# Optimization experiments

Measured on AMD Instinct MI355X. Metric: run time of the kernel, lower is better.

The kernel has to match this reference:

```python
import jax, jax.numpy as jnp
import numpy as np

NF = 96   # out_channel_M
G = 8     # deformable groups
K = 3     # deform conv kernel size


def conv2d(x, w, b, stride=1, pad=1):
    out = jax.lax.conv_general_dilated(x, w, (stride, stride), [(pad, pad), (pad, pad)],
                                       dimension_numbers=('NCHW', 'OIHW', 'NCHW'))
    return out + b[None, :, None, None]


def conv_transpose2d(x, w, b, stride=2, pad=1, out_pad=1):
    # PyTorch ConvTranspose2d semantics; w is [Cin, Cout, k, k]
    k = w.shape[2]
    wt = jnp.flip(w, (2, 3)).transpose(1, 0, 2, 3)  # -> OIHW
    p = (k - 1 - pad, k - 1 - pad + out_pad)
    out = jax.lax.conv_general_dilated(x, wt, (1, 1), [p, p], lhs_dilation=(stride, stride),
                                       dimension_numbers=('NCHW', 'OIHW', 'NCHW'))
    return out + b[None, :, None, None]


def lrelu(x):
    return jax.nn.leaky_relu(x, 0.1)


def deform_conv(x, offset, w, b):
    """DCNv1: offset-driven bilinear sampling + 3x3 contraction (stride=1, pad=1).
    x: [B,C,H,W], offset: [B, 2*G*K*K, H, W] (per-group (dy,dx) interleaved per tap)."""
    B, C, H, W = x.shape
    K2 = K * K
    Cg = C // G
    off = offset.reshape(B, G, K2, 2, H, W)
    ky, kx = jnp.meshgrid(jnp.arange(K), jnp.arange(K), indexing='ij')
    # sampling positions: p = p0 + p_k + delta_p  (zero padding of 1)
    py = (jnp.arange(H, dtype=x.dtype)[None, None, None, :, None]
          + (ky.reshape(K2) - 1).astype(x.dtype)[None, None, :, None, None] + off[:, :, :, 0])
    px = (jnp.arange(W, dtype=x.dtype)[None, None, None, None, :]
          + (kx.reshape(K2) - 1).astype(x.dtype)[None, None, :, None, None] + off[:, :, :, 1])
    y0 = jnp.floor(py); x0 = jnp.floor(px)
    ly = py - y0; lx = px - x0
    y0i = y0.astype(jnp.int32); x0i = x0.astype(jnp.int32)
    xg = x.reshape(B, G, Cg, H * W)  # channels within a deformable group share offsets

    def gather(yi, xi):
        valid = ((yi >= 0) & (yi < H) & (xi >= 0) & (xi < W)).astype(x.dtype)  # [B,G,K2,H,W]
        idx = jnp.clip(yi, 0, H - 1) * W + jnp.clip(xi, 0, W - 1)
        g = jnp.take_along_axis(xg, idx.reshape(B, G, 1, K2 * H * W), axis=3)
        return g.reshape(B, G, Cg, K2, H, W) * valid[:, :, None]

    bw = lambda a: a[:, :, None]  # broadcast bilinear weight over channel axis
    v = (gather(y0i, x0i) * bw((1 - ly) * (1 - lx))
         + gather(y0i, x0i + 1) * bw((1 - ly) * lx)
         + gather(y0i + 1, x0i) * bw(ly * (1 - lx))
         + gather(y0i + 1, x0i + 1) * bw(ly * lx))
    sampled = v.reshape(B, C, K2, H, W)
    out = jnp.einsum('bckhw,ock->bohw', sampled, w.reshape(w.shape[0], C, K2))
    return out + b[None, :, None, None]


def setup_inputs():
    key = jax.random.key(0)
    ks = jax.random.split(key, 16)
    B, H, W = 2, 128, 128
    s = 0.05
    wgt = lambda k, shape: jax.random.normal(k, shape, jnp.float32) * s
    return {
        'ref_fea': jax.random.normal(ks[0], (B, NF, H, W), jnp.float32),
        'inp_fea': jax.random.normal(ks[1], (B, NF, H, W), jnp.float32),
        'oc1_w': wgt(ks[2], (NF, 2 * NF, 3, 3)), 'oc1_b': jnp.zeros((NF,), jnp.float32),
        'oc3_w': wgt(ks[3], (NF, NF, 3, 3)), 'oc3_b': jnp.zeros((NF,), jnp.float32),
        'enc1_w': wgt(ks[4], (NF, NF, 3, 3)), 'enc1_b': jnp.zeros((NF,), jnp.float32),
        'enc2_w': wgt(ks[5], (NF, NF, 3, 3)), 'enc2_b': jnp.zeros((NF,), jnp.float32),
        'dec1_w': wgt(ks[6], (NF, NF, 3, 3)), 'dec1_b': jnp.zeros((NF,), jnp.float32),
        'dec2_w': wgt(ks[7], (NF, NF, 3, 3)), 'dec2_b': jnp.zeros((NF,), jnp.float32),
        'coff_w': wgt(ks[8], (2 * G * K * K, NF, 3, 3)), 'coff_b': jnp.zeros((2 * G * K * K,), jnp.float32),
        'dcn_w': wgt(ks[9], (NF, NF, 3, 3)), 'dcn_b': jnp.zeros((NF,), jnp.float32),
        'ref1_w': wgt(ks[10], (NF, 2 * NF, 3, 3)), 'ref1_b': jnp.zeros((NF,), jnp.float32),
        'ref2_w': wgt(ks[11], (NF, NF, 3, 3)), 'ref2_b': jnp.zeros((NF,), jnp.float32),
    }


def reference(ref_fea, inp_fea, oc1_w, oc1_b, oc3_w, oc3_b, enc1_w, enc1_b, enc2_w, enc2_b,
              dec1_w, dec1_b, dec2_w, dec2_b, coff_w, coff_b, dcn_w, dcn_b,
              ref1_w, ref1_b, ref2_w, ref2_b):
    # MotionEstimation
    t = jnp.concatenate([ref_fea, inp_fea], axis=1)
    t = lrelu(conv2d(t, oc1_w, oc1_b))
    t = lrelu(conv2d(t, oc3_w, oc3_b))
    en_offset = conv2d(lrelu(conv2d(t, enc1_w, enc1_b, stride=2)), enc2_w, enc2_b, stride=2)
    # Q: round-to-integer quantization (straight-through; same forward value as round)
    q_offset = en_offset + jax.lax.stop_gradient(jnp.round(en_offset) - en_offset)
    # MotionCompensation
    de_offset = conv_transpose2d(lrelu(conv_transpose2d(q_offset, dec1_w, dec1_b)), dec2_w, dec2_b)
    offset = conv2d(de_offset, coff_w, coff_b)  # conv_offset inside DCNv1 (extra_offset_mask)
    aligned = deform_conv(ref_fea, offset, dcn_w, dcn_b)
    r = lrelu(conv2d(jnp.concatenate([aligned, ref_fea], axis=1), ref1_w, ref1_b))
    r = lrelu(conv2d(r, ref2_w, ref2_b))
    return aligned + r, en_offset, q_offset
```

## Files before the change

### kernel.cpp

```cpp
#include <hip/hip_runtime.h>
#include <hip/hip_bf16.h>

typedef __hip_bfloat16 bf16;
typedef __attribute__((ext_vector_type(8))) short s8;
typedef __attribute__((ext_vector_type(4))) short s4;
typedef __attribute__((ext_vector_type(4))) float f4;

#define N_FEA   3145728
#define N_EN    196608
#define N_E1    786432
#define OUT_EN  3145728
#define OUT_Q   3342336

__device__ __forceinline__ float b2f(bf16 v) { return __bfloat162float(v); }
__device__ __forceinline__ float bs2f(short v) {
    union { unsigned u; float f; } x; x.u = ((unsigned)(unsigned short)v) << 16; return x.f;
}

__global__ void wpack_sw(const float* __restrict__ w1, const float* __restrict__ w3,
                         float* __restrict__ o1, float* __restrict__ o3) {
    long i = (long)blockIdx.x * 256 + threadIdx.x;
    const long n1 = 2L * 12 * 96 * 72;
    if (i < n1) {
        int ky = (int)(i % 3); long t = i / 3;
        int o = (int)(t % 8); t /= 8;
        int kx = (int)(t % 3); t /= 3;
        int c = (int)(t % 96); t /= 96;
        int ocg = (int)(t % 12); int ks = (int)(t / 12);
        o1[i] = w1[((long)(ocg * 8 + o) * 192 + ks * 96 + c) * 9 + ky * 3 + kx];
        return;
    }
    i -= n1;
    const long n3 = 2L * 12 * 48 * 72;
    if (i < n3) {
        int ky = (int)(i % 3); long t = i / 3;
        int o = (int)(t % 8); t /= 8;
        int kx = (int)(t % 3); t /= 3;
        int c = (int)(t % 48); t /= 48;
        int ocg = (int)(t % 12); int ks = (int)(t / 12);
        o3[i] = w3[((long)(ocg * 8 + o) * 96 + ks * 48 + c) * 9 + ky * 3 + kx];
    }
}

__global__ void wpack_enc(const float* __restrict__ w1, const float* __restrict__ w2,
                          float* __restrict__ o1, float* __restrict__ o2) {
    long i = (long)blockIdx.x * 256 + threadIdx.x;
    const long n1 = 24L * 96 * 4 * 9;
    if (i < n1) {
        int k = (int)(i % 9);
        int o = (int)((i / 9) % 4);
        int c = (int)((i / 36) % 96);
        int ocg = (int)(i / (36 * 96));
        o1[i] = w1[((long)(ocg * 4 + o) * 96 + c) * 9 + k];
        return;
    }
    i -= n1;
    const long n2 = 48L * 96 * 2 * 9;
    if (i < n2) {
        int k = (int)(i % 9);
        int o = (int)((i / 9) % 2);
        int c = (int)((i / 18) % 96);
        int ocg = (int)(i / (18 * 96));
        o2[i] = w2[((long)(ocg * 2 + o) * 96 + c) * 9 + k];
    }
}

template <int OCB>
__global__ __launch_bounds__(256) void conv3x3_sw(
    const float* __restrict__ inA, int cA, int bstrA,
    const float* __restrict__ inB, int cB, int bstrB,
    const float* __restrict__ wsc,
    float* __restrict__ P0, float* __restrict__ P1, int Cout) {
    const int H = 128, W = 128;
    const int NOC = Cout / OCB;
    int bid = blockIdx.x;
    const int ks = bid & 1;
    int r = bid >> 1;
    const int strip = r & 15; r >>= 4;
    const int ocg = r % NOC;
    const int b = r / NOC;
    const float* in = ks ? inB : inA;
    const int cN = ks ? cB : cA;
    const int bstr = ks ? bstrB : bstrA;
    float* P = ks ? P1 : P0;
    const float* wq0 = wsc + ((long)(ks * NOC + ocg) * cN) * 72;

    const int ox = threadIdx.x & 127;
    const int ry = (threadIdx.x >> 7) << 2;
    const int oy0 = strip * 8 + ry;
    const int iyb = oy0 - 1;

    bool vy[6];
#pragma unroll
    for (int j = 0; j < 6; ++j) vy[j] = (unsigned)(iyb + j) < (unsigned)H;

    float acc[OCB][4];
#pragma unroll
    for (int o = 0; o < OCB; ++o)
#pragma unroll
        for (int j = 0; j < 4; ++j) acc[o][j] = 0.f;

    const float* pc = in + (long)b * bstr * H * W + (long)iyb * W;
    for (int c = 0; c < cN; ++c) {
        const float* wq = wq0 + c * 72;
#pragma unroll
        for (int kx = 0; kx < 3; ++kx) {
            const int ix = ox + kx - 1;
            const bool vx = (unsigned)ix < (unsigned)W;
            float rv[6];
#pragma unroll
            for (int j = 0; j < 6; ++j)
                rv[j] = (vx && vy[j]) ? pc[j * W + ix] : 0.f;
#pragma unroll
            for (int o = 0; o < OCB; ++o) {
#pragma unroll
                for (int ky = 0; ky < 3; ++ky) {
                    float wz = wq[kx * 24 + o * 3 + ky];
#pragma unroll
                    for (int j = 0; j < 4; ++j)
                        acc[o][j] = fmaf(rv[j + ky], wz, acc[o][j]);
                }
            }
        }
        pc += (long)H * W;
    }
#pragma unroll
    for (int o = 0; o < OCB; ++o) {
        long base = (((long)b * Cout + ocg * OCB + o) * H + oy0) * W + ox;
#pragma unroll
        for (int j = 0; j < 4; ++j) P[base + (long)j * W] = acc[o][j];
    }
}

__global__ void fuse_add_k(const float* __restrict__ p0, const float* __restrict__ p1,
                           const float* __restrict__ bias, float* __restrict__ out) {
    long idx = (long)blockIdx.x * 256 + threadIdx.x;
    if (idx >= (long)N_FEA) return;
    int oc = (int)((idx >> 14) % 96);
    float a = bias[oc] + p0[idx] + p1[idx];
    out[idx] = a > 0.f ? a : 0.1f * a;
}

template <int OCB>
__global__ __launch_bounds__(256) void conv_s2_px(
    const float* __restrict__ in, int Cin, int Hin, int Win,
    const float* __restrict__ wsc, const float* __restrict__ bias,
    float* __restrict__ out, int Cout, int relu,
    float* __restrict__ qq, float* __restrict__ qf2) {
    const int Hout = Hin >> 1, Wout = Win >> 1;
    const int rpb = 256 / Wout;
    const int strips = Hout / rpb;
    int bid = blockIdx.x;
    const int strip = bid % strips; bid /= strips;
    const int NOC = Cout / OCB;
    const int ocg = bid % NOC;
    const int b = bid / NOC;
    const int tid = threadIdx.x;
    const int ox = tid % Wout;
    const int oy = strip * rpb + tid / Wout;
    const int iy0 = oy * 2 - 1, ix0 = ox * 2 - 1;
    const float* wq0 = wsc + (long)(ocg * Cin) * (OCB * 9);

    float acc[OCB];
#pragma unroll
    for (int o = 0; o < OCB; ++o) acc[o] = bias[ocg * OCB + o];
    const bool vx0 = ix0 >= 0;
    const bool vy0 = iy0 >= 0;

    const float* pc = in + (long)b * Cin * Hin * Win + (long)iy0 * Win + ix0;
    for (int c = 0; c < Cin; ++c) {
        float rv[3][3];
#pragma unroll
        for (int jr = 0; jr < 3; ++jr) {
            const float* row = pc + jr * Win;
            const bool vr = jr ? true : vy0;
            rv[jr][0] = (vr && vx0) ? row[0] : 0.f;
            rv[jr][1] = vr ? row[1] : 0.f;
            rv[jr][2] = vr ? row[2] : 0.f;
        }
        const float* wq = wq0 + c * (OCB * 9);
#pragma unroll
        for (int o = 0; o < OCB; ++o)
#pragma unroll
            for (int ky = 0; ky < 3; ++ky)
#pragma unroll
                for (int kx = 0; kx < 3; ++kx)
                    acc[o] = fmaf(rv[ky][kx], wq[o * 9 + ky * 3 + kx], acc[o]);
        pc += (long)Hin * Win;
    }
#pragma unroll
    for (int o = 0; o < OCB; ++o) {
        long idx = (((long)b * Cout + ocg * OCB + o) * Hout + oy) * Wout + ox;
        float a = acc[o];
        if (relu) a = a > 0.f ? a : 0.1f * a;
        out[idx] = a;
        if (qq) {
            float qv = rintf(a);
            qq[idx] = qv;
            qf2[idx] = qv;
        }
    }
}

template <int HWC>
__global__ __launch_bounds__(256) void convt3x3_v2(
    const float* __restrict__ in, const float* __restrict__ w,
    const float* __restrict__ bias, void* __restrict__ out,
    int Hin, int Win, int relu) {
    const int C = 96;
    const int Hout = 2 * Hin, Wout = 2 * Win;
    const int strips = (Hout * Wout) / 1024;
    int bid = blockIdx.x;
    const int strip = bid % strips; bid /= strips;
    const int oc = bid % C;
    const int b = bid / C;
    __shared__ float wl[864];
    for (int i = threadIdx.x; i < C * 9; i += 256) {
        int c = i / 9, k = i % 9;
        wl[i] = w[((long)c * C + oc) * 9 + k];
    }
    __syncthreads();
    const int pix = strip * 1024 + threadIdx.x * 4;
    const int oy = pix / Wout, oxb = pix % Wout;
    const int c0x = oxb >> 1;
    const int oyE = oy + 1;
    float acc[4];
    const float bz = bias[oc];
#pragma unroll
    for (int j = 0; j < 4; ++j) acc[j] = bz;
    const bool r2ok = (c0x + 2) < Win;

    const float* pl = in + (long)b * C * Hin * Win;
    for (int c = 0; c < C; ++c) {
        float wv[9];
#pragma unroll
        for (int k = 0; k < 9; ++k) wv[k] = wl[c * 9 + k];
#pragma unroll
        for (int ky = 0; ky < 3; ++ky) {
            int ty = oyE - ky;
            if (ty & 1) continue;
            int iy = ty >> 1;
            if ((unsigned)iy >= (unsigned)Hin) continue;
            const float* row = pl + (long)iy * Win + c0x;
            float r0 = row[0];
            float r1 = row[1];
            float r2 = r2ok ? row[2] : 0.f;
            acc[0] = fmaf(r0, wv[ky * 3 + 1], acc[0]);
            acc[1] = fmaf(r1, wv[ky * 3 + 0], acc[1]);
            acc[1] = fmaf(r0, wv[ky * 3 + 2], acc[1]);
            acc[2] = fmaf(r1, wv[ky * 3 + 1], acc[2]);
            acc[3] = fmaf(r2, wv[ky * 3 + 0], acc[3]);
            acc[3] = fmaf(r1, wv[ky * 3 + 2], acc[3]);
        }
        pl += (long)Hin * Win;
    }
#pragma unroll
    for (int j = 0; j < 4; ++j) {
        float a = acc[j];
        if (relu) a = a > 0.f ? a : 0.1f * a;
        if (HWC)
            ((bf16*)out)[((long)b * Hout * Wout + oy * Wout + oxb + j) * 96 + oc] =
                __float2bfloat16(a);
        else
            ((float*)out)[(((long)b * C + oc) * Hout + oy) * Wout + oxb + j] = a;
    }
}

__device__ __forceinline__ void packw(const float* __restrict__ w, bf16* __restrict__ wP,
                                      int Cin, int swap, long i) {
    const int cpt = Cin >> 5;
    int e = (int)(i & 7);
    int n16 = (int)((i >> 3) & 15);
    int q = (int)((i >> 7) & 3);
    long t = i >> 9;
    int ci = (int)(t % cpt); t /= cpt;
    int tap = (int)(t % 9);
    int g = (int)(t / 9);
    int oc = g * 16 + n16;
    int c = ci * 32 + q * 8 + e;
    int cs = swap ? (c + Cin / 2) % Cin : c;
    wP[i] = __float2bfloat16(w[((long)oc * Cin + cs) * 9 + tap]);
}
__global__ void wxform_all(const float* __restrict__ coffw, const float* __restrict__ ref1w,
                           const float* __restrict__ ref2w, const float* __restrict__ dcnw,
                           bf16* __restrict__ p_coff, bf16* __restrict__ p_ref1,
                           bf16* __restrict__ p_ref2, bf16* __restrict__ p_dcn) {
    const long n1 = 124416, n2 = 165888, n3 = 82944, n4 = 82944;
    long i = (long)blockIdx.x * 256 + threadIdx.x;
    if (i < n1) { packw(coffw, p_coff, 96, 0, i); return; }
    i -= n1;
    if (i < n2) { packw(ref1w, p_ref1, 192, 1, i); return; }
    i -= n2;
    if (i < n3) { packw(ref2w, p_ref2, 96, 0, i); return; }
    i -= n3;
    if (i < n4) {
        int e = (int)(i & 7);
        int n16 = (int)((i >> 3) & 15);
        int q = (int)((i >> 7) & 3);
        long t = i >> 9;
        int ci = (int)(t % 27);
        int g = (int)(t / 27);
        int kp = ci * 32 + q * 8 + e;
        int c = kp % 96, kk = kp / 96;
        p_dcn[i] = __float2bfloat16(dcnw[(long)(g * 16 + n16) * 864 + c * 9 + kk]);
    }
}

__global__ void pack_hwc(const float* __restrict__ src, bf16* __restrict__ dst,
                         int HW, int Cs, int coff) {
    long i = (long)blockIdx.x * 256 + threadIdx.x;
    if (i >= 2L * 96 * HW) return;
    int px = (int)(i % HW);
    long t = i / HW;
    int c = (int)(t % 96);
    int b = (int)(t / 96);
    dst[((long)b * HW + px) * Cs + coff + c] = __float2bfloat16(src[i]);
}

template <int EPI>
__global__ __launch_bounds__(256) void mconv(
    const bf16* __restrict__ X, const bf16* __restrict__ wP,
    const float* __restrict__ bias, void* __restrict__ out,
    const bf16* __restrict__ res,
    int Cin, int Cout, int H, int W, int relu) {
    const int HW = H * W;
    const int NG = Cout >> 4, split = (NG + 1) >> 1;
    int bid = blockIdx.x;
    const int nb = HW >> 6;
    const int pxb = (bid % nb) << 6;
    const int b = bid / nb;
    const int wave = threadIdx.x >> 6, lane = threadIdx.x & 63;
    const int mt = (wave >> 1) << 5;
    const int og0 = (wave & 1) ? split : 0;
    const int og1 = (wave & 1) ? NG : split;
    const int q = lane >> 4, n16 = lane & 15;
    const int pA0 = pxb + mt + n16, pA1 = pA0 + 16;
    const int oy0 = pA0 / W, ox0 = pA0 % W;
    const int oy1 = pA1 / W, ox1 = pA1 % W;
    const long ib = (long)b * HW * Cin;
    f4 acc0[5], acc1[5];
    const f4 z4 = {0.f, 0.f, 0.f, 0.f};
#pragma unroll
    for (int g = 0; g < 5; ++g) { acc0[g] = z4; acc1[g] = z4; }
    const s8 z8 = {0, 0, 0, 0, 0, 0, 0, 0};
    const int cpt = Cin >> 5;
    const int lofs = lane << 3;
    for (int tap = 0; tap < 9; ++tap) {
        const int ky = tap / 3 - 1, kx = tap % 3 - 1;
        const int iy0 = oy0 + ky, ix0 = ox0 + kx;
        const int iy1 = oy1 + ky, ix1 = ox1 + kx;
        const bool v0 = (unsigned)iy0 < (unsigned)H && (unsigned)ix0 < (unsigned)W;
        const bool v1 = (unsigned)iy1 < (unsigned)H && (unsigned)ix1 < (unsigned)W;
        const bf16* pa0 = X + ib + ((long)iy0 * W + ix0) * Cin + q * 8;
        const bf16* pa1 = X + ib + ((long)iy1 * W + ix1) * Cin + q * 8;
        for (int ci = 0; ci < cpt; ++ci) {
            const int c0 = ci << 5;
            s8 a0 = v0 ? *(const s8*)(pa0 + c0) : z8;
            s8 a1 = v1 ? *(const s8*)(pa1 + c0) : z8;
#pragma unroll
            for (int gi = 0; gi < 5; ++gi) {
                int g = og0 + gi;
                if (g >= og1) break;
                s8 bb = *(const s8*)(wP + ((long)(g * 9 + tap) * cpt + ci) * 512 + lofs);
                acc0[gi] = __builtin_amdgcn_mfma_f32_16x16x32_bf16(a0, bb, acc0[gi], 0, 0, 0);
                acc1[gi] = __builtin_amdgcn_mfma_f32_16x16x32_bf16(a1, bb, acc1[gi], 0, 0, 0);
            }
        }
    }
#pragma unroll
    for (int gi = 0; gi < 5; ++gi) {
        int g = og0 + gi;
        if (g >= og1) break;
        int oc = g * 16 + n16;
        float bz = bias[oc];
#pragma unroll
        for (int t = 0; t < 2; ++t) {
            f4 a = t ? acc1[gi] : acc0[gi];
            int pxl = pxb + mt + t * 16 + q * 4;
#pragma unroll
            for (int r = 0; r < 4; ++r) {
                float v = a[r] + bz;
                if (relu) v = v > 0.f ? v : 0.1f * v;
                int px = pxl + r;
                if (EPI == 0)
                    ((bf16*)out)[((long)b * HW + px) * Cout + oc] = __float2bfloat16(v);
                else {
                    v += b2f(res[((long)b * HW + px) * 192 + 96 + oc]);
                    ((float*)out)[((long)b * Cout + oc) * HW + px] = v;
                }
            }
        }
    }
}

__global__ __launch_bounds__(256, 4) void deform_m_k(
    const bf16* __restrict__ Xref, const bf16* __restrict__ offs,
    const bf16* __restrict__ wD, const float* __restrict__ db,
    bf16* __restrict__ X2) {
    const int H = 128, W = 128;
    __shared__ bf16 offL[16 * 144];
    __shared__ bf16 s[16][872];
    int bid = blockIdx.x;
    const int band = bid & 7;
    int r = bid >> 3;
    const int b = r >> 7; r &= 127;
    const int rowin = r >> 3, xb = r & 7;
    const int oy = band * 16 + rowin;
    const int ox0 = xb * 16;
    const int tid = threadIdx.x;
    const long pxbase = (long)b * (H * W) + oy * W + ox0;
    for (int e = tid; e < 16 * 144; e += 256)
        offL[e] = offs[(pxbase + (e / 144)) * 144 + (e % 144)];
    __syncthreads();
    const long refb = (long)b * (H * W);
    for (int e = tid; e < 16 * 72; e += 256) {
        int p = e / 72, rem = e % 72;
        int g8 = rem / 9, kk = rem % 9;
        int ox = ox0 + p;
        float offy = b2f(offL[p * 144 + g8 * 18 + kk * 2]);
        float offx = b2f(offL[p * 144 + g8 * 18 + kk * 2 + 1]);
        float py = (float)(oy + kk / 3 - 1) + offy;
        float px = (float)(ox + kk % 3 - 1) + offx;
        float y0f = floorf(py), x0f = floorf(px);
        float ly = py - y0f, lx = px - x0f;
        int y0 = (int)y0f, x0 = (int)x0f;
        float w00 = (1.f - ly) * (1.f - lx), w01 = (1.f - ly) * lx;
        float w10 = ly * (1.f - lx), w11 = ly * lx;
        float v[12];
#pragma unroll
        for (int j = 0; j < 12; ++j) v[j] = 0.f;
        auto corner = [&](int yy, int xx, float wgt) {
            if ((unsigned)yy < (unsigned)H && (unsigned)xx < (unsigned)W) {
                const s4* cp = (const s4*)(Xref + (refb + yy * W + xx) * 192 + g8 * 12);
                s4 c0 = cp[0], c1 = cp[1], c2 = cp[2];
#pragma unroll
                for (int j = 0; j < 4; ++j) {
                    v[j]     = fmaf(bs2f(c0[j]), wgt, v[j]);
                    v[4 + j] = fmaf(bs2f(c1[j]), wgt, v[4 + j]);
                    v[8 + j] = fmaf(bs2f(c2[j]), wgt, v[8 + j]);
                }
            }
        };
        corner(y0, x0, w00);
        corner(y0, x0 + 1, w01);
        corner(y0 + 1, x0, w10);
        corner(y0 + 1, x0 + 1, w11);
        short rr[12];
#pragma unroll
        for (int j = 0; j < 12; ++j) {
            bf16 h = __float2bfloat16(v[j]);
            rr[j] = *(short*)&h;
        }
        s4* dst = (s4*)&s[p][kk * 96 + g8 * 12];
        dst[0] = ((s4*)rr)[0];
        dst[1] = ((s4*)rr)[1];
        dst[2] = ((s4*)rr)[2];
    }
    __syncthreads();
    const int wave = tid >> 6, lane = tid & 63;
    const int q = lane >> 4, n16 = lane & 15;
    const f4 z4 = {0.f, 0.f, 0.f, 0.f};
    for (int g = wave; g < 6; g += 4) {
        f4 acc = z4;
        const bf16* wg = wD + (long)g * 27 * 512 + (lane << 3);
#pragma unroll 3
        for (int ci = 0; ci < 27; ++ci) {
            s8 a = *(const s8*)&s[n16][ci * 32 + q * 8];
            s8 bb = *(const s8*)(wg + ci * 512);
            acc = __builtin_amdgcn_mfma_f32_16x16x32_bf16(a, bb, acc, 0, 0, 0);
        }
        int oc = g * 16 + n16;
        float bz = db[oc];
#pragma unroll
        for (int rr2 = 0; rr2 < 4; ++rr2) {
            int p = q * 4 + rr2;
            X2[(pxbase + p) * 192 + 96 + oc] = __float2bfloat16(acc[rr2] + bz);
        }
    }
}

extern "C" void kernel_launch(void* const* d_in, const int* in_sizes, int n_in,
                              void* d_out, int out_size, void* d_ws, size_t ws_size,
                              hipStream_t stream) {
    const float* ref_fea = (const float*)d_in[0];
    const float* inp_fea = (const float*)d_in[1];
    const float* oc1_w = (const float*)d_in[2];  const float* oc1_b = (const float*)d_in[3];
    const float* oc3_w = (const float*)d_in[4];  const float* oc3_b = (const float*)d_in[5];
    const float* enc1_w = (const float*)d_in[6]; const float* enc1_b = (const float*)d_in[7];
    const float* enc2_w = (const float*)d_in[8]; const float* enc2_b = (const float*)d_in[9];
    const float* dec1_w = (const float*)d_in[10]; const float* dec1_b = (const float*)d_in[11];
    const float* dec2_w = (const float*)d_in[12]; const float* dec2_b = (const float*)d_in[13];
    const float* coff_w = (const float*)d_in[14]; const float* coff_b = (const float*)d_in[15];
    const float* dcn_w = (const float*)d_in[16];  const float* dcn_b = (const float*)d_in[17];
    const float* ref1_w = (const float*)d_in[18]; const float* ref1_b = (const float*)d_in[19];
    const float* ref2_w = (const float*)d_in[20]; const float* ref2_b = (const float*)d_in[21];

    float* out = (float*)d_out;
    float* OUTS = out;
    float* S1 = (float*)d_ws;
    float* S2 = S1 + N_FEA;
    float* F = S1 + N_E1;
    bf16* de_hwc = (bf16*)S1;
    bf16* offs = (bf16*)S2;
    bf16* X2 = (bf16*)S1;
    bf16* r1 = (bf16*)S2;
    bf16* wtb = (bf16*)S2 + 4800000;
    bf16* wt_coff = wtb;
    bf16* wt_ref1 = wt_coff + 124416;
    bf16* wt_ref2 = wt_ref1 + 165888;
    bf16* wt_dcn = wt_ref2 + 82944;
    float* wsc1 = out + OUT_EN;
    float* wsc3 = wsc1 + 165888;
    float* wenc1 = S1 + 1048576;
    float* wenc2 = wenc1 + 82944;

    dim3 blk(256);
    auto nb = [](long n) { return dim3((unsigned)((n + 255) / 256)); };

    wpack_sw<<<nb(165888L + 82944), blk, 0, stream>>>(oc1_w, oc3_w, wsc1, wsc3);
    conv3x3_sw<8><<<dim3(768), blk, 0, stream>>>(ref_fea, 96, 96,
                                                 inp_fea, 96, 96,
                                                 wsc1, S1, S2, 96);
    fuse_add_k<<<nb(N_FEA), blk, 0, stream>>>(S1, S2, oc1_b, OUTS);
    conv3x3_sw<8><<<dim3(768), blk, 0, stream>>>(OUTS, 48, 96,
                                                 OUTS + 48 * 16384, 48, 96,
                                                 wsc3, S1, S2, 96);
    fuse_add_k<<<nb(N_FEA), blk, 0, stream>>>(S1, S2, oc3_b, OUTS);
    wpack_enc<<<nb(82944L + 82944), blk, 0, stream>>>(enc1_w, enc2_w, wenc1, wenc2);
    conv_s2_px<4><<<dim3(768), blk, 0, stream>>>(OUTS, 96, 128, 128,
                                                 wenc1, enc1_b, S1, 96, 1,
                                                 nullptr, nullptr);
    wxform_all<<<nb(124416L + 165888 + 82944 + 82944), blk, 0, stream>>>(
        coff_w, ref1_w, ref2_w, dcn_w, wt_coff, wt_ref1, wt_ref2, wt_dcn);
    conv_s2_px<2><<<dim3(384), blk, 0, stream>>>(S1, 96, 64, 64,
                                                 wenc2, enc2_b, out + OUT_EN, 96, 0,
                                                 out + OUT_Q, F);
    convt3x3_v2<0><<<dim3(2 * 96 * 4), blk, 0, stream>>>(F, dec1_w, dec1_b, S2, 32, 32, 1);
    convt3x3_v2<1><<<dim3(2 * 96 * 16), blk, 0, stream>>>(S2, dec2_w, dec2_b, de_hwc,
                                                          64, 64, 0);
    mconv<0><<<dim3(512), blk, 0, stream>>>(de_hwc, wt_coff, coff_b, offs, nullptr,
                                            96, 144, 128, 128, 0);
    pack_hwc<<<nb(N_FEA), blk, 0, stream>>>(ref_fea, X2, 16384, 192, 0);
    deform_m_k<<<dim3(2048), blk, 0, stream>>>(X2, offs, wt_dcn, dcn_b, X2);
    mconv<0><<<dim3(512), blk, 0, stream>>>(X2, wt_ref1, ref1_b, r1, nullptr,
                                            192, 96, 128, 128, 1);
    mconv<3><<<dim3(512), blk, 0, stream>>>(r1, wt_ref2, ref2_b, out, X2,
                                            96, 96, 128, 128, 1);
}
```

Before: 931.1 us.

## Restructure transposed convs to per-input-pixel quads with multi-channel output blocking

Replaces the per-output-channel transposed conv kernel with one where each thread owns one input pixel and writes its 2x2 output quad, computing OCB output channels at once from pre-packed weights. Each input value loaded is reused across several output channels and all four sub-pixel phases, and the parity branches disappear. A new weight-pack kernel reorders the decoder weights, adding one more small launch. Weights are now read directly from global memory instead of shared memory, and per-thread register use grows with OCB.

```diff
diff --git a/kernel.cpp b/kernel.cpp
--- a/kernel.cpp
+++ b/kernel.cpp
@@ -62,6 +62,29 @@
         int c = (int)((i / 18) % 96);
         int ocg = (int)(i / (18 * 96));
         o2[i] = w2[((long)(ocg * 2 + o) * 96 + c) * 9 + k];
+    }
+}
+
+__global__ void wpack_dec(const float* __restrict__ w1, const float* __restrict__ w2,
+                          float* __restrict__ o1, float* __restrict__ o2) {
+    long i = (long)blockIdx.x * 256 + threadIdx.x;
+    const long n1 = 48L * 96 * 2 * 9;
+    if (i < n1) {
+        int k = (int)(i % 9);
+        int o = (int)((i / 9) % 2);
+        int c = (int)((i / 18) % 96);
+        int ocg = (int)(i / (18 * 96));
+        o1[i] = w1[((long)c * 96 + ocg * 2 + o) * 9 + k];
+        return;
+    }
+    i -= n1;
+    const long n2 = 24L * 96 * 4 * 9;
+    if (i < n2) {
+        int k = (int)(i % 9);
+        int o = (int)((i / 9) % 4);
+        int c = (int)((i / 36) % 96);
+        int ocg = (int)(i / (36 * 96));
+        o2[i] = w2[((long)c * 96 + ocg * 4 + o) * 9 + k];
     }
 }
 
@@ -202,67 +225,65 @@
     }
 }
 
-template <int HWC>
-__global__ __launch_bounds__(256) void convt3x3_v2(
-    const float* __restrict__ in, const float* __restrict__ w,
+template <int OCB, int HWC>
+__global__ __launch_bounds__(256) void convt_quad(
+    const float* __restrict__ in, const float* __restrict__ wsc,
     const float* __restrict__ bias, void* __restrict__ out,
     int Hin, int Win, int relu) {
     const int C = 96;
     const int Hout = 2 * Hin, Wout = 2 * Win;
-    const int strips = (Hout * Wout) / 1024;
+    const int strips = (Hin * Win) / 256;
     int bid = blockIdx.x;
     const int strip = bid % strips; bid /= strips;
-    const int oc = bid % C;
-    const int b = bid / C;
-    __shared__ float wl[864];
-    for (int i = threadIdx.x; i < C * 9; i += 256) {
-        int c = i / 9, k = i % 9;
-        wl[i] = w[((long)c * C + oc) * 9 + k];
-    }
-    __syncthreads();
-    const int pix = strip * 1024 + threadIdx.x * 4;
-    const int oy = pix / Wout, oxb = pix % Wout;
-    const int c0x = oxb >> 1;
-    const int oyE = oy + 1;
-    float acc[4];
-    const float bz = bias[oc];
-#pragma unroll
-    for (int j = 0; j < 4; ++j) acc[j] = bz;
-    const bool r2ok = (c0x + 2) < Win;
-
-    const float* pl = in + (long)b * C * Hin * Win;
+    const int NOC = C / OCB;
+    const int ocg = bid % NOC;
+    const int b = bid / NOC;
+    const int idx = strip * 256 + threadIdx.x;
+    const int iy = idx / Win, ix = idx % Win;
+    const bool vr = (ix + 1) < Win, vd = (iy + 1) < Hin;
+    const float* wq0 = wsc + (long)(ocg * C) * (OCB * 9);
+
+    float acc[OCB][4];
+#pragma unroll
+    for (int o = 0; o < OCB; ++o) {
+        float bz = bias[ocg * OCB + o];
+#pragma unroll
+        for (int j = 0; j < 4; ++j) acc[o][j] = bz;
+    }
+    const float* pc = in + (long)b * C * Hin * Win + (long)iy * Win + ix;
     for (int c = 0; c < C; ++c) {
-        float wv[9];
-#pragma unroll
-        for (int k = 0; k < 9; ++k) wv[k] = wl[c * 9 + k];
-#pragma unroll
-        for (int ky = 0; ky < 3; ++ky) {
-            int ty = oyE - ky;
-            if (ty & 1) continue;
-            int iy = ty >> 1;
-            if ((unsigned)iy >= (unsigned)Hin) continue;
-            const float* row = pl + (long)iy * Win + c0x;
-            float r0 = row[0];
-            float r1 = row[1];
-            float r2 = r2ok ? row[2] : 0.f;
-            acc[0] = fmaf(r0, wv[ky * 3 + 1], acc[0]);
-            acc[1] = fmaf(r1, wv[ky * 3 + 0], acc[1]);
-            acc[1] = fmaf(r0, wv[ky * 3 + 2], acc[1]);
-            acc[2] = fmaf(r1, wv[ky * 3 + 1], acc[2]);
-            acc[3] = fmaf(r2, wv[ky * 3 + 0], acc[3]);
-            acc[3] = fmaf(r1, wv[ky * 3 + 2], acc[3]);
-        }
-        pl += (long)Hin * Win;
-    }
-#pragma unroll
-    for (int j = 0; j < 4; ++j) {
-        float a = acc[j];
-        if (relu) a = a > 0.f ? a : 0.1f * a;
-        if (HWC)
-            ((bf16*)out)[((long)b * Hout * Wout + oy * Wout + oxb + j) * 96 + oc] =
-                __float2bfloat16(a);
-        else
-            ((float*)out)[(((long)b * C + oc) * Hout + oy) * Wout + oxb + j] = a;
+        float i00 = pc[0];
+        float i01 = vr ? pc[1] : 0.f;
+        float i10 = vd ? pc[Win] : 0.f;
+        float i11 = (vr && vd) ? pc[Win + 1] : 0.f;
+        const float* wq = wq0 + c * (OCB * 9);
+#pragma unroll
+        for (int o = 0; o < OCB; ++o) {
+            const float* w = wq + o * 9;
+            acc[o][0] = fmaf(i00, w[4], acc[o][0]);
+            acc[o][1] = fmaf(i01, w[3], fmaf(i00, w[5], acc[o][1]));
+            acc[o][2] = fmaf(i10, w[1], fmaf(i00, w[7], acc[o][2]));
+            acc[o][3] = fmaf(i11, w[0],
+                        fmaf(i10, w[2],
+                        fmaf(i01, w[6],
+                        fmaf(i00, w[8], acc[o][3]))));
+        }
+        pc += (long)Hin * Win;
+    }
+#pragma unroll
+    for (int o = 0; o < OCB; ++o) {
+        int oc = ocg * OCB + o;
+#pragma unroll
+        for (int j = 0; j < 4; ++j) {
+            float a = acc[o][j];
+            if (relu) a = a > 0.f ? a : 0.1f * a;
+            int oy = 2 * iy + (j >> 1), ox2 = 2 * ix + (j & 1);
+            if (HWC)
+                ((bf16*)out)[((long)b * Hout * Wout + (long)oy * Wout + ox2) * 96 + oc] =
+                    __float2bfloat16(a);
+            else
+                ((float*)out)[(((long)b * C + oc) * Hout + oy) * Wout + ox2] = a;
+        }
     }
 }
 
@@ -509,6 +530,8 @@
     bf16* wt_ref1 = wt_coff + 124416;
     bf16* wt_ref2 = wt_ref1 + 165888;
     bf16* wt_dcn = wt_ref2 + 82944;
+    float* wdec1 = (float*)(wt_dcn + 82944);
+    float* wdec2 = wdec1 + 82944;
     float* wsc1 = out + OUT_EN;
     float* wsc3 = wsc1 + 165888;
     float* wenc1 = S1 + 1048576;
@@ -532,12 +555,12 @@
                                                  nullptr, nullptr);
     wxform_all<<<nb(124416L + 165888 + 82944 + 82944), blk, 0, stream>>>(
         coff_w, ref1_w, ref2_w, dcn_w, wt_coff, wt_ref1, wt_ref2, wt_dcn);
+    wpack_dec<<<nb(82944L + 82944), blk, 0, stream>>>(dec1_w, dec2_w, wdec1, wdec2);
     conv_s2_px<2><<<dim3(384), blk, 0, stream>>>(S1, 96, 64, 64,
                                                  wenc2, enc2_b, out + OUT_EN, 96, 0,
                                                  out + OUT_Q, F);
-    convt3x3_v2<0><<<dim3(2 * 96 * 4), blk, 0, stream>>>(F, dec1_w, dec1_b, S2, 32, 32, 1);
-    convt3x3_v2<1><<<dim3(2 * 96 * 16), blk, 0, stream>>>(S2, dec2_w, dec2_b, de_hwc,
-                                                          64, 64, 0);
+    convt_quad<2, 0><<<dim3(384), blk, 0, stream>>>(F, wdec1, dec1_b, S2, 32, 32, 1);
+    convt_quad<4, 1><<<dim3(768), blk, 0, stream>>>(S2, wdec2, dec2_b, de_hwc, 64, 64, 0);
     mconv<0><<<dim3(512), blk, 0, stream>>>(de_hwc, wt_coff, coff_b, offs, nullptr,
                                             96, 144, 128, 128, 0);
     pack_hwc<<<nb(N_FEA), blk, 0, stream>>>(ref_fea, X2, 16384, 192, 0);
```

Result: faster. 769.0 us (-17.4%).
